# Kernel optimization log

Hardware: AMD Instinct MI355X
Metric: run time of the kernel (lower is better)

## Reference

```python
import jax, jax.numpy as jnp
import numpy as np

B, NPG, H, HEADS, L, E, IN_DIM, FREQ = 4, 256, 128, 4, 6, 65536, 5, 256
N = B * NPG
C = H // HEADS  # per-head channels = 32


def _w(key, shape, fan_in):
    return jax.random.normal(key, shape, jnp.float32) * (fan_in ** -0.5)


def _ln(x):  # LayerNorm, elementwise_affine=False, eps=1e-5
    mu = jnp.mean(x, axis=-1, keepdims=True)
    var = jnp.mean((x - mu) ** 2, axis=-1, keepdims=True)
    return (x - mu) / jnp.sqrt(var + 1e-5)


def setup_inputs() -> dict:
    key = jax.random.key(0)
    ks = jax.random.split(key, 40)
    x = jax.random.normal(ks[0], (N, IN_DIM), jnp.float32)
    # edges constrained within each graph
    kg = jnp.repeat(jnp.arange(B), E // B)
    src = jax.random.randint(ks[1], (E,), 0, NPG) + kg * NPG
    dst = jax.random.randint(ks[2], (E,), 0, NPG) + kg * NPG
    edge_index = jnp.stack([src, dst]).astype(jnp.int32)
    batch = jnp.repeat(jnp.arange(B), NPG).astype(jnp.int32)
    time_matrix = jax.random.normal(ks[3], (N, N), jnp.float32)
    p = {}
    p['Wn'] = _w(ks[4], (IN_DIM, H), IN_DIM); p['bn'] = jnp.zeros((H,), jnp.float32)
    p['Wee'] = _w(ks[5], (1, 1), 1); p['bee'] = jnp.zeros((1,), jnp.float32)
    p['Wt1'] = _w(ks[6], (FREQ, H), FREQ); p['bt1'] = jnp.zeros((H,), jnp.float32)
    p['Wt2'] = _w(ks[7], (H, H), H); p['bt2'] = jnp.zeros((H,), jnp.float32)
    p['Wa'] = _w(ks[8], (L, H, 4 * H), H); p['ba'] = jnp.zeros((L, 4 * H), jnp.float32)
    p['Wq'] = _w(ks[9], (L, H, H), H); p['bq'] = jnp.zeros((L, H), jnp.float32)
    p['Wk'] = _w(ks[10], (L, H, H), H); p['bk'] = jnp.zeros((L, H), jnp.float32)
    p['Wv'] = _w(ks[11], (L, H, H), H); p['bv'] = jnp.zeros((L, H), jnp.float32)
    p['We'] = _w(ks[12], (L, 1, H), 1)  # lin_edge, bias=False in PyG
    p['Wskip'] = _w(ks[13], (L, H, H), H); p['bskip'] = jnp.zeros((L, H), jnp.float32)
    p['Wf1'] = _w(ks[14], (L, H, 2 * H), H); p['bf1'] = jnp.zeros((L, 2 * H), jnp.float32)
    p['Wf2'] = _w(ks[15], (L, 2 * H, H), 2 * H); p['bf2'] = jnp.zeros((L, H), jnp.float32)
    p['Wb'] = _w(ks[16], (H, H, H), H); p['bb'] = jnp.zeros((H,), jnp.float32)
    p['Wm1'] = _w(ks[17], (H, H), H); p['bm1'] = jnp.zeros((H,), jnp.float32)
    p['Wm2'] = _w(ks[18], (H, 4), H); p['bm2'] = jnp.zeros((4,), jnp.float32)
    return {'x': x, 'edge_index': edge_index, 'batch': batch, 't': 50,
            'time_matrix': time_matrix, **p}


def reference(x, edge_index, batch, t, time_matrix,
              Wn, bn, Wee, bee, Wt1, bt1, Wt2, bt2,
              Wa, ba, Wq, bq, Wk, bk, Wv, bv, We, Wskip, bskip,
              Wf1, bf1, Wf2, bf2, Wb, bb, Wm1, bm1, Wm2, bm2):
    h = x @ Wn + bn  # [N,H]
    # sinusoidal timestep embedding (dim=FREQ)
    half = FREQ // 2
    freqs = jnp.exp(-jnp.log(jnp.float32(10000.0)) * jnp.arange(half, dtype=jnp.float32) / half)
    targs = jnp.float32(t) * freqs
    emb = jnp.concatenate([jnp.cos(targs), jnp.sin(targs)])[None, :]  # [1,FREQ]
    t_emb = jax.nn.silu(emb @ Wt1 + bt1) @ Wt2 + bt2  # [1,H]
    t_mod = jax.nn.silu(t_emb)

    src, dst = edge_index[0], edge_index[1]
    edge_attr = time_matrix[src, dst][:, None] @ Wee + bee  # [E,1]

    inv_sqrt_c = jnp.float32(1.0 / np.sqrt(C))
    for l in range(L):
        ss = t_mod @ Wa[l] + ba[l]  # [1,4H]
        sh_msa, sc_msa, sh_mlp, sc_mlp = jnp.split(ss, 4, axis=1)
        hn = _ln(h) * (1 + sc_msa) + sh_msa
        # TransformerConv: gather per-edge Q/K/V, softmax over incoming edges of dst
        q = (hn @ Wq[l] + bq[l]).reshape(N, HEADS, C)
        k = (hn @ Wk[l] + bk[l]).reshape(N, HEADS, C)
        v = (hn @ Wv[l] + bv[l]).reshape(N, HEADS, C)
        e = (edge_attr @ We[l]).reshape(E, HEADS, C)
        kj = k[src] + e
        alpha = jnp.sum(q[dst] * kj, axis=-1) * inv_sqrt_c  # [E,HEADS]
        m = jax.ops.segment_max(alpha, dst, num_segments=N)
        a = jnp.exp(alpha - m[dst])
        s = jax.ops.segment_sum(a, dst, num_segments=N)
        a = a / (s[dst] + 1e-16)
        msg = (v[src] + e) * a[..., None]  # [E,HEADS,C]
        attn_out = jax.ops.segment_sum(msg, dst, num_segments=N).reshape(N, H)
        attn_out = attn_out + hn @ Wskip[l] + bskip[l]  # root/skip connection
        h = h + attn_out
        hn = _ln(h) * (1 + sc_mlp) + sh_mlp
        h = h + (jax.nn.gelu(hn @ Wf1[l] + bf1[l], approximate=False) @ Wf2[l] + bf2[l])

    # to_dense_batch: all graphs have NPG nodes -> reshape, full mask
    hd = h.reshape(B, NPG, H)
    # nn.Bilinear: pair[b,i,j,o] = h[b,i] @ Wb[o] @ h[b,j] + bb[o]
    tmp = jnp.einsum('bik,okl->biol', hd, Wb)  # [B,n,H,H]
    pair = jnp.einsum('biol,bjl->bijo', tmp, hd) + bb  # [B,n,n,H]
    logits = jax.nn.silu(pair @ Wm1 + bm1) @ Wm2 + bm2  # [B,n,n,4]
    return logits
```

## Files before the change

kernel.cpp:

```cpp
#include <hip/hip_runtime.h>
#include <math.h>

#define N_NODES 1024
#define HDIM 128
#define EDGES 65536
#define LAYERS 6

typedef __attribute__((ext_vector_type(8))) short bf16x8;
typedef __attribute__((ext_vector_type(4))) float f32x4;

#define OFF_H     0
#define OFF_Q     131072
#define OFF_K     262144
#define OFF_V     393216
#define OFF_SKP   524288
#define OFF_G     655360
#define OFF_SS    917504
#define OFF_EA    920576
#define OFF_CVEC  986112
#define OFF_INT   986240
#define OFF_M     1054912
#define OFF_U     3152064
#define OFF_MT    11540672
#define OFF_HB    12589248
#define OFF_TMOD  12654784
#define OFF_WB    12654912

#define WM1T_OFF  786432

__device__ __forceinline__ float silu_f(float x) { return x / (1.f + expf(-x)); }
__device__ __forceinline__ float frcp(float x) { return __builtin_amdgcn_rcpf(x); }

__device__ __forceinline__ unsigned short f2bf(float f) {
    unsigned int u = __float_as_uint(f);
    u += 0x7FFFu + ((u >> 16) & 1u);
    return (unsigned short)(u >> 16);
}

__global__ __launch_bounds__(256) void k_ssf(const void* tptr,
    const float* __restrict__ Wt1, const float* __restrict__ bt1,
    const float* __restrict__ Wt2, const float* __restrict__ bt2,
    const float* __restrict__ bb, const float* __restrict__ Wm1, const float* __restrict__ bm1,
    const float* __restrict__ Wa, const float* __restrict__ ba,
    float* __restrict__ ss_all, float* __restrict__ cvec)
{
    __shared__ float emb_s[256];
    __shared__ float part[2][128];
    __shared__ float tmp1_s[128];
    __shared__ float tmod_s[128];
    int tid = threadIdx.x;
    int iv = *(const int*)tptr;
    float fv = __int_as_float(iv);
    float tval = (iv > -1000000 && iv < 1000000) ? (float)iv : fv;
    {
        int fi = tid & 127;
        float fr = expf(-logf(10000.f) * (float)fi / 128.f);
        float ta = tval * fr;
        emb_s[tid] = (tid < 128) ? cosf(ta) : sinf(ta);
    }
    __syncthreads();
    {
        int col = tid & 127, sl = tid >> 7;
        float p = 0.f;
#pragma unroll 8
        for (int i = sl * 128; i < sl * 128 + 128; i++) p += emb_s[i] * Wt1[i * 128 + col];
        part[sl][col] = p;
    }
    __syncthreads();
    if (tid < 128) tmp1_s[tid] = silu_f(bt1[tid] + part[0][tid] + part[1][tid]);
    __syncthreads();
    {
        int col = tid & 127, sl = tid >> 7;
        float p = 0.f;
#pragma unroll 8
        for (int i = sl * 64; i < sl * 64 + 64; i++) p += tmp1_s[i] * Wt2[i * 128 + col];
        part[sl][col] = p;
    }
    __syncthreads();
    if (tid < 128) tmod_s[tid] = silu_f(bt2[tid] + part[0][tid] + part[1][tid]);
    __syncthreads();
    {
        int idx = blockIdx.x * 256 + tid;
        int l = idx >> 9, j = idx & 511;
        float a = ba[l * 512 + j];
        const float* w = Wa + l * 65536 + j;
#pragma unroll 4
        for (int k = 0; k < 128; k++) a += tmod_s[k] * w[k * 512];
        ss_all[idx] = a;
    }
    if (blockIdx.x == 0) {
        {
            int col = tid & 127, sl = tid >> 7;
            float p = 0.f;
#pragma unroll 8
            for (int i = sl * 64; i < sl * 64 + 64; i++) p += bb[i] * Wm1[i * 128 + col];
            part[sl][col] = p;
        }
        __syncthreads();
        if (tid < 128) cvec[tid] = bm1[tid] + part[0][tid] + part[1][tid];
    }
}

__global__ __launch_bounds__(256) void k_wtrans(
    const float* __restrict__ Wq, const float* __restrict__ Wk,
    const float* __restrict__ Wv, const float* __restrict__ Wsk,
    const float* __restrict__ Wf1, const float* __restrict__ Wf2,
    const float* __restrict__ Wm1, short* __restrict__ WT)
{
    __shared__ __align__(16) short T[64][80];
    int t = blockIdx.x;
    int tid = threadIdx.x;
    const float* src; short* dst; int K, N, kt, nt;
    if (t < 96) {
        int mat = t >> 2, sub = t & 3;
        int l = mat >> 2, m = mat & 3;
        src = (m == 0 ? Wq : m == 1 ? Wk : m == 2 ? Wv : Wsk) + l * 16384;
        dst = WT + (size_t)mat * 16384;
        K = 128; N = 128; kt = sub >> 1; nt = sub & 1;
    } else if (t < 144) {
        int i = t - 96; int l = i >> 3, sub = i & 7;
        src = Wf1 + l * 32768;
        dst = WT + 24 * 16384 + (size_t)l * 32768;
        K = 128; N = 256; kt = sub & 1; nt = sub >> 1;
    } else if (t < 192) {
        int i = t - 144; int l = i >> 3, sub = i & 7;
        src = Wf2 + l * 32768;
        dst = WT + 24 * 16384 + 6 * 32768 + (size_t)l * 32768;
        K = 256; N = 128; kt = sub >> 1; nt = sub & 1;
    } else {
        int sub = t - 192;
        src = Wm1;
        dst = WT + WM1T_OFF;
        K = 128; N = 128; kt = sub >> 1; nt = sub & 1;
    }
    int k0 = kt * 64, n0 = nt * 64;
    for (int p = 0; p < 16; p++) {
        int idx = p * 256 + tid;
        int kk = idx >> 6, nn = idx & 63;
        T[nn][kk] = (short)f2bf(src[(k0 + kk) * N + n0 + nn]);
    }
    __syncthreads();
    for (int p = 0; p < 2; p++) {
        int idx = p * 256 + tid;
        int nn = idx >> 3, sq = idx & 7;
        *(int4*)&dst[(size_t)(n0 + nn) * K + k0 + sq * 8] = *(const int4*)&T[nn][sq * 8];
    }
}

__global__ __launch_bounds__(256) void k_inpedge(const float* __restrict__ x,
    const float* __restrict__ Wn, const float* __restrict__ bn, float* __restrict__ h,
    const int* __restrict__ ei, const float* __restrict__ tm,
    const float* __restrict__ Wee, const float* __restrict__ bee,
    float* __restrict__ ea, int* __restrict__ deg)
{
    int bid = blockIdx.x;
    int tid = threadIdx.x;
    if (bid < 512) {
        int idx = bid * 256 + tid;
        int i = idx >> 7, j = idx & 127;
        float acc = bn[j];
#pragma unroll
        for (int kk = 0; kk < 5; kk++) acc += x[i * 5 + kk] * Wn[kk * 128 + j];
        h[idx] = acc;
    } else {
        int e = (bid - 512) * 256 + tid;
        int s = ei[e], d = ei[EDGES + e];
        ea[e] = tm[s * N_NODES + d] * Wee[0] + bee[0];
        atomicAdd(&deg[d], 1);
    }
}

__global__ __launch_bounds__(1024) void k_scan(const int* __restrict__ deg, int* __restrict__ rowptr)
{
    __shared__ int tmp[1024];
    int tid = threadIdx.x;
    tmp[tid] = deg[tid];
    __syncthreads();
    for (int off = 1; off < 1024; off <<= 1) {
        int vv = (tid >= off) ? tmp[tid - off] : 0;
        __syncthreads();
        tmp[tid] += vv;
        __syncthreads();
    }
    rowptr[tid + 1] = tmp[tid];
    if (tid == 0) rowptr[0] = 0;
}

__global__ __launch_bounds__(256) void k_scatter(const int* __restrict__ ei,
    const int* __restrict__ rowptr, int* __restrict__ cursor, int* __restrict__ eorder)
{
    int e = blockIdx.x * 256 + threadIdx.x;
    int d = ei[EDGES + e];
    int pos = atomicAdd(&cursor[d], 1);
    eorder[rowptr[d] + pos] = e;
}

__global__ __launch_bounds__(128) void k_sort2(const int* __restrict__ rowptr,
    int* __restrict__ eorder, const int* __restrict__ ei, const float* __restrict__ ea,
    int* __restrict__ src_csr, float* __restrict__ ea_csr)
{
    __shared__ int key[256];
    int node = blockIdx.x;
    int tid = threadIdx.x;
    int beg = rowptr[node], end = rowptr[node + 1];
    int n = end - beg;
    if (n <= 256) {
        for (int i = tid; i < 256; i += 128) key[i] = (i < n) ? eorder[beg + i] : 0x7FFFFFFF;
        __syncthreads();
        for (int k = 2; k <= 256; k <<= 1) {
            for (int j = k >> 1; j > 0; j >>= 1) {
                int i = ((tid / j) * 2 * j) + (tid % j);
                int l = i + j;
                bool up = ((i & k) == 0);
                int a = key[i], b = key[l];
                if ((a > b) == up) { key[i] = b; key[l] = a; }
                __syncthreads();
            }
        }
        for (int i = tid; i < n; i += 128) {
            int e = key[i];
            src_csr[beg + i] = ei[e];
            ea_csr[beg + i] = ea[e];
        }
    } else {
        if (tid == 0) {
            for (int i = beg + 1; i < end; ++i) {
                int kk = eorder[i];
                int j = i - 1;
                while (j >= beg && eorder[j] > kk) { eorder[j + 1] = eorder[j]; --j; }
                eorder[j + 1] = kk;
            }
        }
        __syncthreads();
        for (int i = tid; i < n; i += 128) {
            int e = eorder[beg + i];
            src_csr[beg + i] = ei[e];
            ea_csr[beg + i] = ea[e];
        }
    }
}

__global__ __launch_bounds__(256) void k_qkvs(const float* __restrict__ h,
    const float* __restrict__ ss, const short* __restrict__ WT, int layer,
    const float* __restrict__ bq, const float* __restrict__ bk,
    const float* __restrict__ bv, const float* __restrict__ bsk,
    float* __restrict__ q, float* __restrict__ k, float* __restrict__ v, float* __restrict__ skp)
{
    __shared__ __align__(16) short As[32][136];
    __shared__ float shs[128], scs[128];
    int tid = threadIdx.x;
    int r0 = blockIdx.x * 32;
    int mat = blockIdx.y;
    if (tid < 128) { shs[tid] = ss[tid]; scs[tid] = ss[128 + tid]; }
    __syncthreads();
    {
        int row = tid >> 3, o = tid & 7;
        const float* hr = h + (size_t)(r0 + row) * 128 + o * 16;
        float s = 0.f, s2 = 0.f;
#pragma unroll
        for (int j = 0; j < 4; j++) {
            float4 vv = *(const float4*)&hr[j * 4];
            s += vv.x + vv.y + vv.z + vv.w;
            s2 += vv.x * vv.x + vv.y * vv.y + vv.z * vv.z + vv.w * vv.w;
        }
        s += __shfl_xor(s, 1, 64); s2 += __shfl_xor(s2, 1, 64);
        s += __shfl_xor(s, 2, 64); s2 += __shfl_xor(s2, 2, 64);
        s += __shfl_xor(s, 4, 64); s2 += __shfl_xor(s2, 4, 64);
        float mu = s * (1.f / 128.f);
        float var = s2 * (1.f / 128.f) - mu * mu;
        float rs = rsqrtf(var + 1e-5f);
#pragma unroll
        for (int j = 0; j < 4; j++) {
            float4 vv = *(const float4*)&hr[j * 4];
            int cb = o * 16 + j * 4;
            short4 o4;
            o4.x = (short)f2bf((vv.x - mu) * rs * (1.f + scs[cb])     + shs[cb]);
            o4.y = (short)f2bf((vv.y - mu) * rs * (1.f + scs[cb + 1]) + shs[cb + 1]);
            o4.z = (short)f2bf((vv.z - mu) * rs * (1.f + scs[cb + 2]) + shs[cb + 2]);
            o4.w = (short)f2bf((vv.w - mu) * rs * (1.f + scs[cb + 3]) + shs[cb + 3]);
            *(short4*)&As[row][cb] = o4;
        }
    }
    __syncthreads();
    int w = tid >> 6, lane = tid & 63, c = lane & 15, g = lane >> 4;
    const short* Wm = WT + (size_t)(layer * 4 + mat) * 16384;
    f32x4 acc[2][2] = {};
#pragma unroll
    for (int kq = 0; kq < 4; kq++) {
        int ko = kq * 32 + g * 8;
        bf16x8 a0 = *(const bf16x8*)&As[c][ko];
        bf16x8 a1 = *(const bf16x8*)&As[16 + c][ko];
#pragma unroll
        for (int nt = 0; nt < 2; nt++) {
            bf16x8 bfr = *(const bf16x8*)&Wm[(size_t)(w * 32 + nt * 16 + c) * 128 + ko];
            acc[0][nt] = __builtin_amdgcn_mfma_f32_16x16x32_bf16(a0, bfr, acc[0][nt], 0, 0, 0);
            acc[1][nt] = __builtin_amdgcn_mfma_f32_16x16x32_bf16(a1, bfr, acc[1][nt], 0, 0, 0);
        }
    }
    const float* bias; float* out;
    switch (mat) {
        case 0:  bias = bq;  out = q;   break;
        case 1:  bias = bk;  out = k;   break;
        case 2:  bias = bv;  out = v;   break;
        default: bias = bsk; out = skp; break;
    }
#pragma unroll
    for (int it = 0; it < 2; it++)
#pragma unroll
        for (int nt = 0; nt < 2; nt++) {
            int n = w * 32 + nt * 16 + c;
            float bv2 = bias[n];
#pragma unroll
            for (int r = 0; r < 4; r++) {
                int i = r0 + it * 16 + g * 4 + r;
                out[(size_t)i * 128 + n] = acc[it][nt][r] + bv2;
            }
        }
}

__global__ __launch_bounds__(256) void k_ffn(float* __restrict__ h,
    const short* __restrict__ WT, int layer,
    const float* __restrict__ bf1, const float* __restrict__ bf2,
    const float* __restrict__ ss2, short* __restrict__ hb, int last)
{
    __shared__ __align__(16) short As[16][136];
    __shared__ __align__(16) short Gs[16][264];
    __shared__ float shs[128], scs[128];
    int tid = threadIdx.x;
    int r0 = blockIdx.x * 16;
    if (tid < 128) { shs[tid] = ss2[tid]; scs[tid] = ss2[128 + tid]; }
    __syncthreads();
    {
        int row = tid >> 4, o = tid & 15;
        const float* hr = h + (size_t)(r0 + row) * 128 + o * 8;
        float s = 0.f, s2 = 0.f;
#pragma unroll
        for (int j = 0; j < 2; j++) {
            float4 vv = *(const float4*)&hr[j * 4];
            s += vv.x + vv.y + vv.z + vv.w;
            s2 += vv.x * vv.x + vv.y * vv.y + vv.z * vv.z + vv.w * vv.w;
        }
        s += __shfl_xor(s, 1, 64); s2 += __shfl_xor(s2, 1, 64);
        s += __shfl_xor(s, 2, 64); s2 += __shfl_xor(s2, 2, 64);
        s += __shfl_xor(s, 4, 64); s2 += __shfl_xor(s2, 4, 64);
        s += __shfl_xor(s, 8, 64); s2 += __shfl_xor(s2, 8, 64);
        float mu = s * (1.f / 128.f);
        float var = s2 * (1.f / 128.f) - mu * mu;
        float rs = rsqrtf(var + 1e-5f);
#pragma unroll
        for (int j = 0; j < 2; j++) {
            float4 vv = *(const float4*)&hr[j * 4];
            int cb = o * 8 + j * 4;
            short4 o4;
            o4.x = (short)f2bf((vv.x - mu) * rs * (1.f + scs[cb])     + shs[cb]);
            o4.y = (short)f2bf((vv.y - mu) * rs * (1.f + scs[cb + 1]) + shs[cb + 1]);
            o4.z = (short)f2bf((vv.z - mu) * rs * (1.f + scs[cb + 2]) + shs[cb + 2]);
            o4.w = (short)f2bf((vv.w - mu) * rs * (1.f + scs[cb + 3]) + shs[cb + 3]);
            *(short4*)&As[row][cb] = o4;
        }
    }
    __syncthreads();
    int w = tid >> 6, lane = tid & 63, c = lane & 15, g = lane >> 4;
    const short* W1 = WT + 24 * 16384 + (size_t)layer * 32768;
    const short* W2 = WT + 24 * 16384 + 6 * 32768 + (size_t)layer * 32768;
    {
        f32x4 acc[4] = {};
#pragma unroll
        for (int kq = 0; kq < 4; kq++) {
            int ko = kq * 32 + g * 8;
            bf16x8 a0 = *(const bf16x8*)&As[c][ko];
#pragma unroll
            for (int nt = 0; nt < 4; nt++) {
                bf16x8 bfr = *(const bf16x8*)&W1[(size_t)(w * 64 + nt * 16 + c) * 128 + ko];
                acc[nt] = __builtin_amdgcn_mfma_f32_16x16x32_bf16(a0, bfr, acc[nt], 0, 0, 0);
            }
        }
#pragma unroll
        for (int nt = 0; nt < 4; nt++) {
            int n = w * 64 + nt * 16 + c;
            float bv = bf1[n];
#pragma unroll
            for (int r = 0; r < 4; r++) {
                float y = acc[nt][r] + bv;
                float gl = 0.5f * y * (1.f + erff(y * 0.70710678118654752f));
                Gs[g * 4 + r][n] = (short)f2bf(gl);
            }
        }
    }
    __syncthreads();
    {
        f32x4 acc2[2] = {};
#pragma unroll
        for (int kq = 0; kq < 8; kq++) {
            int ko = kq * 32 + g * 8;
            bf16x8 a0 = *(const bf16x8*)&Gs[c][ko];
#pragma unroll
            for (int nt2 = 0; nt2 < 2; nt2++) {
                bf16x8 bfr = *(const bf16x8*)&W2[(size_t)(w * 32 + nt2 * 16 + c) * 256 + ko];
                acc2[nt2] = __builtin_amdgcn_mfma_f32_16x16x32_bf16(a0, bfr, acc2[nt2], 0, 0, 0);
            }
        }
#pragma unroll
        for (int nt2 = 0; nt2 < 2; nt2++) {
            int n = w * 32 + nt2 * 16 + c;
            float bv = bf2[n];
#pragma unroll
            for (int r = 0; r < 4; r++) {
                int i = r0 + g * 4 + r;
                float nv = h[(size_t)i * 128 + n] + acc2[nt2][r] + bv;
                h[(size_t)i * 128 + n] = nv;
                if (last) hb[(size_t)i * 128 + n] = (short)f2bf(nv);
            }
        }
    }
}

__global__ __launch_bounds__(256) void k_attn(const float* __restrict__ q,
    const float* __restrict__ k, const float* __restrict__ v,
    const float* __restrict__ skp, float* __restrict__ h,
    const int* __restrict__ src_csr, const float* __restrict__ ea_csr,
    const float* __restrict__ We_l, const int* __restrict__ rowptr)
{
    __shared__ float ms[3][64], ssb[3][64], a0s[3][64], a1s[3][64];
    int tid = threadIdx.x;
    int wid = tid >> 6;
    int lane = tid & 63;
    int node = blockIdx.x;
    int c0 = lane * 2;
    float2 q2 = *(const float2*)&q[node * 128 + c0];
    float we0 = We_l[c0], we1 = We_l[c0 + 1];
    int beg = rowptr[node], end = rowptr[node + 1];
    int n = end - beg;
    int tb = beg + (n * wid) / 4;
    int te = beg + (n * (wid + 1)) / 4;
    float m = -INFINITY, s = 0.f, a0 = 0.f, a1 = 0.f;
    const float isc = 0.17677669529663687f;

    int t = tb;
    for (; t + 3 < te; t += 4) {
        int sn0 = src_csr[t],     sn1 = src_csr[t + 1];
        int sn2 = src_csr[t + 2], sn3 = src_csr[t + 3];
        float e0 = ea_csr[t],     e1 = ea_csr[t + 1];
        float e2 = ea_csr[t + 2], e3 = ea_csr[t + 3];
        float2 k0 = *(const float2*)&k[sn0 * 128 + c0];
        float2 k1 = *(const float2*)&k[sn1 * 128 + c0];
        float2 k2 = *(const float2*)&k[sn2 * 128 + c0];
        float2 k3 = *(const float2*)&k[sn3 * 128 + c0];
        float2 v0 = *(const float2*)&v[sn0 * 128 + c0];
        float2 v1 = *(const float2*)&v[sn1 * 128 + c0];
        float2 v2 = *(const float2*)&v[sn2 * 128 + c0];
        float2 v3 = *(const float2*)&v[sn3 * 128 + c0];
        float p0 = q2.x * (k0.x + e0 * we0) + q2.y * (k0.y + e0 * we1);
        float p1 = q2.x * (k1.x + e1 * we0) + q2.y * (k1.y + e1 * we1);
        float p2 = q2.x * (k2.x + e2 * we0) + q2.y * (k2.y + e2 * we1);
        float p3 = q2.x * (k3.x + e3 * we0) + q2.y * (k3.y + e3 * we1);
        p0 += __shfl_xor(p0, 1, 16); p1 += __shfl_xor(p1, 1, 16);
        p2 += __shfl_xor(p2, 1, 16); p3 += __shfl_xor(p3, 1, 16);
        p0 += __shfl_xor(p0, 2, 16); p1 += __shfl_xor(p1, 2, 16);
        p2 += __shfl_xor(p2, 2, 16); p3 += __shfl_xor(p3, 2, 16);
        p0 += __shfl_xor(p0, 4, 16); p1 += __shfl_xor(p1, 4, 16);
        p2 += __shfl_xor(p2, 4, 16); p3 += __shfl_xor(p3, 4, 16);
        p0 += __shfl_xor(p0, 8, 16); p1 += __shfl_xor(p1, 8, 16);
        p2 += __shfl_xor(p2, 8, 16); p3 += __shfl_xor(p3, 8, 16);
        {
            float al = p0 * isc;
            float mn = fmaxf(m, al);
            float scale = __expf(m - mn), wq = __expf(al - mn);
            s = s * scale + wq;
            a0 = a0 * scale + wq * (v0.x + e0 * we0);
            a1 = a1 * scale + wq * (v0.y + e0 * we1);
            m = mn;
        }
        {
            float al = p1 * isc;
            float mn = fmaxf(m, al);
            float scale = __expf(m - mn), wq = __expf(al - mn);
            s = s * scale + wq;
            a0 = a0 * scale + wq * (v1.x + e1 * we0);
            a1 = a1 * scale + wq * (v1.y + e1 * we1);
            m = mn;
        }
        {
            float al = p2 * isc;
            float mn = fmaxf(m, al);
            float scale = __expf(m - mn), wq = __expf(al - mn);
            s = s * scale + wq;
            a0 = a0 * scale + wq * (v2.x + e2 * we0);
            a1 = a1 * scale + wq * (v2.y + e2 * we1);
            m = mn;
        }
        {
            float al = p3 * isc;
            float mn = fmaxf(m, al);
            float scale = __expf(m - mn), wq = __expf(al - mn);
            s = s * scale + wq;
            a0 = a0 * scale + wq * (v3.x + e3 * we0);
            a1 = a1 * scale + wq * (v3.y + e3 * we1);
            m = mn;
        }
    }
    for (; t < te; ++t) {
        int sn = src_csr[t];
        float eav = ea_csr[t];
        float2 kv = *(const float2*)&k[sn * 128 + c0];
        float2 vv = *(const float2*)&v[sn * 128 + c0];
        float part = q2.x * (kv.x + eav * we0) + q2.y * (kv.y + eav * we1);
        part += __shfl_xor(part, 1, 16);
        part += __shfl_xor(part, 2, 16);
        part += __shfl_xor(part, 4, 16);
        part += __shfl_xor(part, 8, 16);
        float alpha = part * isc;
        float mn = fmaxf(m, alpha);
        float scale = __expf(m - mn), wq = __expf(alpha - mn);
        s = s * scale + wq;
        a0 = a0 * scale + wq * (vv.x + eav * we0);
        a1 = a1 * scale + wq * (vv.y + eav * we1);
        m = mn;
    }
    if (wid > 0) {
        ms[wid - 1][lane] = m; ssb[wid - 1][lane] = s;
        a0s[wid - 1][lane] = a0; a1s[wid - 1][lane] = a1;
    }
    __syncthreads();
    if (wid == 0) {
#pragma unroll
        for (int p = 0; p < 3; p++) {
            float mB = ms[p][lane], sB = ssb[p][lane];
            float b0 = a0s[p][lane], b1 = a1s[p][lane];
            float mm = fmaxf(m, mB);
            float eA = (m  > -1e30f) ? __expf(m  - mm) : 0.f;
            float eB = (mB > -1e30f) ? __expf(mB - mm) : 0.f;
            s = s * eA + sB * eB;
            a0 = a0 * eA + b0 * eB;
            a1 = a1 * eA + b1 * eB;
            m = mm;
        }
        float inv = (s > 0.f) ? 1.f / (s + 1e-16f) : 0.f;
        int o = node * 128 + c0;
        h[o]     += skp[o]     + a0 * inv;
        h[o + 1] += skp[o + 1] + a1 * inv;
    }
}

__global__ __launch_bounds__(256) void k_mprep(const float* __restrict__ Wb,
    const short* __restrict__ WT, float* __restrict__ M)
{
    __shared__ __align__(16) short Bls[128][136];
    int tid = threadIdx.x;
    int k = blockIdx.x;
    const short* Wm1T = WT + WM1T_OFF;
    {
        int lq = (tid & 31) * 4;
        int ob = tid >> 5;
        for (int it = 0; it < 16; it++) {
            int o = it * 8 + ob;
            float4 vv = *(const float4*)&Wb[(size_t)o * 16384 + k * 128 + lq];
            Bls[lq][o]     = (short)f2bf(vv.x);
            Bls[lq + 1][o] = (short)f2bf(vv.y);
            Bls[lq + 2][o] = (short)f2bf(vv.z);
            Bls[lq + 3][o] = (short)f2bf(vv.w);
        }
    }
    __syncthreads();
    int w = tid >> 6, lane = tid & 63, c = lane & 15, g = lane >> 4;
    f32x4 acc[2][8] = {};
#pragma unroll
    for (int kq = 0; kq < 4; kq++) {
        int ko = kq * 32 + g * 8;
        bf16x8 a0 = *(const bf16x8*)&Wm1T[(size_t)(w * 32 + c) * 128 + ko];
        bf16x8 a1 = *(const bf16x8*)&Wm1T[(size_t)(w * 32 + 16 + c) * 128 + ko];
#pragma unroll
        for (int nt = 0; nt < 8; nt++) {
            bf16x8 b = *(const bf16x8*)&Bls[nt * 16 + c][ko];
            acc[0][nt] = __builtin_amdgcn_mfma_f32_16x16x32_bf16(a0, b, acc[0][nt], 0, 0, 0);
            acc[1][nt] = __builtin_amdgcn_mfma_f32_16x16x32_bf16(a1, b, acc[1][nt], 0, 0, 0);
        }
    }
    float* Mk = M + (size_t)k * 16384;
#pragma unroll
    for (int it = 0; it < 2; it++)
#pragma unroll
        for (int nt = 0; nt < 8; nt++)
#pragma unroll
            for (int r = 0; r < 4; r++) {
                int m = w * 32 + it * 16 + g * 4 + r;
                int l = nt * 16 + c;
                Mk[m * 128 + l] = acc[it][nt][r];
            }
}

__global__ __launch_bounds__(256) void k_mtrans(const float* __restrict__ M,
                                                short* __restrict__ Mt)
{
    __shared__ __align__(16) short Ts[64][136];
    int tid = threadIdx.x;
    int n0 = blockIdx.x * 64;
    for (int p = 0; p < 32; p++) {
        int idx = p * 256 + tid;
        int k = idx >> 6, nn = idx & 63;
        Ts[nn][k] = (short)f2bf(M[(size_t)k * 16384 + n0 + nn]);
    }
    __syncthreads();
    for (int p = 0; p < 4; p++) {
        int idx = p * 256 + tid;
        int nn = idx >> 4, s = idx & 15;
        *(int4*)&Mt[(size_t)(n0 + nn) * 128 + s * 8] = *(const int4*)&Ts[nn][s * 8];
    }
}

__global__ __launch_bounds__(256) void k_p1(const short* __restrict__ hb,
    const short* __restrict__ Mt, short* __restrict__ U)
{
    __shared__ __align__(16) short As[128][72];
    __shared__ __align__(16) short Bs[128][72];
    int tid = threadIdx.x;
    int n0 = blockIdx.x * 128;
    int i0 = blockIdx.y * 128;
    int w = tid >> 6, lane = tid & 63, c = lane & 15, g = lane >> 4;
    f32x4 acc[2][8] = {};
    for (int kh = 0; kh < 2; kh++) {
        __syncthreads();
        for (int idx = tid; idx < 1024; idx += 256) {
            int r = idx >> 3, s = idx & 7;
            *(int4*)&As[r][s * 8] = *(const int4*)&hb[(i0 + r) * 128 + kh * 64 + s * 8];
            *(int4*)&Bs[r][s * 8] = *(const int4*)&Mt[(size_t)(n0 + r) * 128 + kh * 64 + s * 8];
        }
        __syncthreads();
#pragma unroll
        for (int kk = 0; kk < 2; kk++) {
            int ko = kk * 32 + g * 8;
            bf16x8 a0 = *(const bf16x8*)&As[w * 32 + c][ko];
            bf16x8 a1 = *(const bf16x8*)&As[w * 32 + 16 + c][ko];
#pragma unroll
            for (int nt = 0; nt < 8; nt++) {
                bf16x8 b = *(const bf16x8*)&Bs[nt * 16 + c][ko];
                acc[0][nt] = __builtin_amdgcn_mfma_f32_16x16x32_bf16(a0, b, acc[0][nt], 0, 0, 0);
                acc[1][nt] = __builtin_amdgcn_mfma_f32_16x16x32_bf16(a1, b, acc[1][nt], 0, 0, 0);
            }
        }
    }
#pragma unroll
    for (int it = 0; it < 2; it++)
#pragma unroll
        for (int nt = 0; nt < 8; nt++)
#pragma unroll
            for (int r = 0; r < 4; r++) {
                int i = i0 + w * 32 + it * 16 + g * 4 + r;
                int n = n0 + nt * 16 + c;
                U[(size_t)i * 16384 + n] = (short)f2bf(acc[it][nt][r]);
            }
}

__global__ __launch_bounds__(256) void k_p2(const short* __restrict__ hb,
    const short* __restrict__ U, const float* __restrict__ cvec,
    const float* __restrict__ Wm2, const float* __restrict__ bm2,
    float* __restrict__ out)
{
    __shared__ __align__(16) short Us[128][136];
    __shared__ float cvs[128];
    __shared__ float w2s[128][4];
    int tid = threadIdx.x;
    int i = blockIdx.x;
    int jb = blockIdx.y;
    int b = i >> 8;
    int w = tid >> 6, lane = tid & 63, c = lane & 15, g = lane >> 4;
    if (tid < 128) {
        cvs[tid] = cvec[tid];
        *(float4*)&w2s[tid][0] = *(const float4*)&Wm2[tid * 4];
    }
    bf16x8 hf[2][4];
    {
        const short* hrow = hb + (size_t)(b * 256 + jb * 128 + w * 32 + c) * 128;
#pragma unroll
        for (int jt = 0; jt < 2; jt++)
#pragma unroll
            for (int kq = 0; kq < 4; kq++)
                hf[jt][kq] = *(const bf16x8*)(hrow + jt * 16 * 128 + kq * 32 + g * 8);
    }
    for (int idx = tid; idx < 2048; idx += 256) {
        int r = idx >> 4, s = idx & 15;
        *(int4*)&Us[r][s * 8] = *(const int4*)&U[(size_t)i * 16384 + r * 128 + s * 8];
    }
    __syncthreads();
    f32x4 acc[2][8] = {};
#pragma unroll
    for (int kq = 0; kq < 4; kq++) {
        int ko = kq * 32 + g * 8;
#pragma unroll
        for (int mt = 0; mt < 8; mt++) {
            bf16x8 uv = *(const bf16x8*)&Us[mt * 16 + c][ko];
            acc[0][mt] = __builtin_amdgcn_mfma_f32_16x16x32_bf16(uv, hf[0][kq], acc[0][mt], 0, 0, 0);
            acc[1][mt] = __builtin_amdgcn_mfma_f32_16x16x32_bf16(uv, hf[1][kq], acc[1][mt], 0, 0, 0);
        }
    }
    float4 bmv = *(const float4*)&bm2[0];
#pragma unroll
    for (int jt = 0; jt < 2; jt++) {
        float p0 = 0.f, p1 = 0.f, p2 = 0.f, p3 = 0.f;
#pragma unroll
        for (int mt = 0; mt < 8; mt++) {
#pragma unroll
            for (int r = 0; r < 4; r++) {
                int m = mt * 16 + g * 4 + r;
                float y = acc[jt][mt][r] + cvs[m];
                float sv = y * frcp(1.f + __expf(-y));
                p0 += sv * w2s[m][0]; p1 += sv * w2s[m][1];
                p2 += sv * w2s[m][2]; p3 += sv * w2s[m][3];
            }
        }
        p0 += __shfl_xor(p0, 16, 64); p1 += __shfl_xor(p1, 16, 64);
        p2 += __shfl_xor(p2, 16, 64); p3 += __shfl_xor(p3, 16, 64);
        p0 += __shfl_xor(p0, 32, 64); p1 += __shfl_xor(p1, 32, 64);
        p2 += __shfl_xor(p2, 32, 64); p3 += __shfl_xor(p3, 32, 64);
        if (g == 0) {
            int j = jb * 128 + w * 32 + jt * 16 + c;
            float4 o4 = { p0 + bmv.x, p1 + bmv.y, p2 + bmv.z, p3 + bmv.w };
            *(float4*)&out[((size_t)i * 256 + j) * 4] = o4;
        }
    }
}

extern "C" void kernel_launch(void* const* d_in, const int* in_sizes, int n_in,
                              void* d_out, int out_size, void* d_ws, size_t ws_size,
                              hipStream_t stream)
{
    const float* x   = (const float*)d_in[0];
    const int*   ei  = (const int*)d_in[1];
    const void*  tptr= d_in[3];
    const float* tm  = (const float*)d_in[4];
    const float* Wn  = (const float*)d_in[5];
    const float* bn  = (const float*)d_in[6];
    const float* Wee = (const float*)d_in[7];
    const float* bee = (const float*)d_in[8];
    const float* Wt1 = (const float*)d_in[9];
    const float* bt1 = (const float*)d_in[10];
    const float* Wt2 = (const float*)d_in[11];
    const float* bt2 = (const float*)d_in[12];
    const float* Wa  = (const float*)d_in[13];
    const float* ba  = (const float*)d_in[14];
    const float* Wq  = (const float*)d_in[15];
    const float* bq  = (const float*)d_in[16];
    const float* Wk  = (const float*)d_in[17];
    const float* bk  = (const float*)d_in[18];
    const float* Wv  = (const float*)d_in[19];
    const float* bv  = (const float*)d_in[20];
    const float* We  = (const float*)d_in[21];
    const float* Wsk = (const float*)d_in[22];
    const float* bsk = (const float*)d_in[23];
    const float* Wf1 = (const float*)d_in[24];
    const float* bf1 = (const float*)d_in[25];
    const float* Wf2 = (const float*)d_in[26];
    const float* bf2 = (const float*)d_in[27];
    const float* Wb  = (const float*)d_in[28];
    const float* bb  = (const float*)d_in[29];
    const float* Wm1 = (const float*)d_in[30];
    const float* bm1 = (const float*)d_in[31];
    const float* Wm2 = (const float*)d_in[32];
    const float* bm2 = (const float*)d_in[33];
    float* out = (float*)d_out;
    float* ws = (float*)d_ws;

    float* h    = ws + OFF_H;
    float* qb   = ws + OFF_Q;
    float* kb   = ws + OFF_K;
    float* vb   = ws + OFF_V;
    float* skp  = ws + OFF_SKP;
    float* ss   = ws + OFF_SS;
    float* ea   = ws + OFF_EA;
    float* cvec = ws + OFF_CVEC;
    int* iws    = (int*)(ws + OFF_INT);
    int* deg    = iws;
    int* cursor = iws + 1024;
    int* rowptr = iws + 2048;
    int* eorder = iws + 3073;
    int* src_csr   = (int*)(ws + OFF_G);
    float* ea_csr  = ws + OFF_G + 65536;
    float* Mst  = ws + OFF_M;
    short* Ub   = (short*)(ws + OFF_U);
    short* Mtb  = (short*)(ws + OFF_MT);
    short* hbb  = (short*)(ws + OFF_HB);
    short* WT   = (short*)(ws + OFF_WB);

    hipMemsetAsync(deg, 0, 2048 * sizeof(int), stream);
    k_ssf<<<12, 256, 0, stream>>>(tptr, Wt1, bt1, Wt2, bt2, bb, Wm1, bm1, Wa, ba, ss, cvec);
    k_wtrans<<<196, 256, 0, stream>>>(Wq, Wk, Wv, Wsk, Wf1, Wf2, Wm1, WT);
    k_inpedge<<<768, 256, 0, stream>>>(x, Wn, bn, h, ei, tm, Wee, bee, ea, deg);
    k_scan<<<1, 1024, 0, stream>>>(deg, rowptr);
    k_scatter<<<256, 256, 0, stream>>>(ei, rowptr, cursor, eorder);
    k_sort2<<<1024, 128, 0, stream>>>(rowptr, eorder, ei, ea, src_csr, ea_csr);

    for (int l = 0; l < LAYERS; l++) {
        const float* ssl = ss + l * 512;
        k_qkvs<<<dim3(32, 4), 256, 0, stream>>>(h, ssl, WT, l,
            bq + l * 128, bk + l * 128, bv + l * 128, bsk + l * 128,
            qb, kb, vb, skp);
        k_attn<<<1024, 256, 0, stream>>>(qb, kb, vb, skp, h, src_csr, ea_csr,
                                         We + l * 128, rowptr);
        k_ffn<<<64, 256, 0, stream>>>(h, WT, l, bf1 + l * 256, bf2 + l * 128,
                                      ssl + 256, hbb, l == LAYERS - 1);
    }

    k_mprep<<<128, 256, 0, stream>>>(Wb, WT, Mst);
    k_mtrans<<<256, 256, 0, stream>>>(Mst, Mtb);
    k_p1<<<dim3(128, 8), 256, 0, stream>>>(hbb, Mtb, Ub);
    k_p2<<<dim3(1024, 2), 256, 0, stream>>>(hbb, Ub, cvec, Wm2, bm2, out);
}
```

Measured before the change: 266.3 us.

## Store K/V in bf16, restructure QKVS blocking and merge P2 column halves

The K and V projections are now written as bf16, and the attention gather reads them as bf16 and widens to float. This halves the gather traffic in the edge loop, at the cost of lower precision in K and V. The QKVS kernel now gives each wave one of the four matrices over 16 rows, instead of using a grid dimension per matrix, so the LayerNorm is computed once per row tile rather than four times. k_p2 drops its second grid dimension: each block loads the U tile once and loops over all 256 columns, removing duplicate U loads at the cost of fewer blocks.

Result: slower. 272.8 us (+2.4%).

```diff
diff --git a/kernel.cpp b/kernel.cpp
--- a/kernel.cpp
+++ b/kernel.cpp
@@ -23,7 +23,6 @@
 #define OFF_U     3152064
 #define OFF_MT    11540672
 #define OFF_HB    12589248
-#define OFF_TMOD  12654784
 #define OFF_WB    12654912
 
 #define WM1T_OFF  786432
@@ -35,6 +34,9 @@
     unsigned int u = __float_as_uint(f);
     u += 0x7FFFu + ((u >> 16) & 1u);
     return (unsigned short)(u >> 16);
+}
+__device__ __forceinline__ float bf2f(unsigned short s) {
+    return __uint_as_float(((unsigned int)s) << 16);
 }
 
 __global__ __launch_bounds__(256) void k_ssf(const void* tptr,
@@ -244,91 +246,14 @@
     const float* __restrict__ ss, const short* __restrict__ WT, int layer,
     const float* __restrict__ bq, const float* __restrict__ bk,
     const float* __restrict__ bv, const float* __restrict__ bsk,
-    float* __restrict__ q, float* __restrict__ k, float* __restrict__ v, float* __restrict__ skp)
-{
-    __shared__ __align__(16) short As[32][136];
+    float* __restrict__ q, short* __restrict__ kb16, short* __restrict__ vb16,
+    float* __restrict__ skp)
+{
+    __shared__ __align__(16) short As[16][136];
     __shared__ float shs[128], scs[128];
     int tid = threadIdx.x;
-    int r0 = blockIdx.x * 32;
-    int mat = blockIdx.y;
+    int r0 = blockIdx.x * 16;
     if (tid < 128) { shs[tid] = ss[tid]; scs[tid] = ss[128 + tid]; }
-    __syncthreads();
-    {
-        int row = tid >> 3, o = tid & 7;
-        const float* hr = h + (size_t)(r0 + row) * 128 + o * 16;
-        float s = 0.f, s2 = 0.f;
-#pragma unroll
-        for (int j = 0; j < 4; j++) {
-            float4 vv = *(const float4*)&hr[j * 4];
-            s += vv.x + vv.y + vv.z + vv.w;
-            s2 += vv.x * vv.x + vv.y * vv.y + vv.z * vv.z + vv.w * vv.w;
-        }
-        s += __shfl_xor(s, 1, 64); s2 += __shfl_xor(s2, 1, 64);
-        s += __shfl_xor(s, 2, 64); s2 += __shfl_xor(s2, 2, 64);
-        s += __shfl_xor(s, 4, 64); s2 += __shfl_xor(s2, 4, 64);
-        float mu = s * (1.f / 128.f);
-        float var = s2 * (1.f / 128.f) - mu * mu;
-        float rs = rsqrtf(var + 1e-5f);
-#pragma unroll
-        for (int j = 0; j < 4; j++) {
-            float4 vv = *(const float4*)&hr[j * 4];
-            int cb = o * 16 + j * 4;
-            short4 o4;
-            o4.x = (short)f2bf((vv.x - mu) * rs * (1.f + scs[cb])     + shs[cb]);
-            o4.y = (short)f2bf((vv.y - mu) * rs * (1.f + scs[cb + 1]) + shs[cb + 1]);
-            o4.z = (short)f2bf((vv.z - mu) * rs * (1.f + scs[cb + 2]) + shs[cb + 2]);
-            o4.w = (short)f2bf((vv.w - mu) * rs * (1.f + scs[cb + 3]) + shs[cb + 3]);
-            *(short4*)&As[row][cb] = o4;
-        }
-    }
-    __syncthreads();
-    int w = tid >> 6, lane = tid & 63, c = lane & 15, g = lane >> 4;
-    const short* Wm = WT + (size_t)(layer * 4 + mat) * 16384;
-    f32x4 acc[2][2] = {};
-#pragma unroll
-    for (int kq = 0; kq < 4; kq++) {
-        int ko = kq * 32 + g * 8;
-        bf16x8 a0 = *(const bf16x8*)&As[c][ko];
-        bf16x8 a1 = *(const bf16x8*)&As[16 + c][ko];
-#pragma unroll
-        for (int nt = 0; nt < 2; nt++) {
-            bf16x8 bfr = *(const bf16x8*)&Wm[(size_t)(w * 32 + nt * 16 + c) * 128 + ko];
-            acc[0][nt] = __builtin_amdgcn_mfma_f32_16x16x32_bf16(a0, bfr, acc[0][nt], 0, 0, 0);
-            acc[1][nt] = __builtin_amdgcn_mfma_f32_16x16x32_bf16(a1, bfr, acc[1][nt], 0, 0, 0);
-        }
-    }
-    const float* bias; float* out;
-    switch (mat) {
-        case 0:  bias = bq;  out = q;   break;
-        case 1:  bias = bk;  out = k;   break;
-        case 2:  bias = bv;  out = v;   break;
-        default: bias = bsk; out = skp; break;
-    }
-#pragma unroll
-    for (int it = 0; it < 2; it++)
-#pragma unroll
-        for (int nt = 0; nt < 2; nt++) {
-            int n = w * 32 + nt * 16 + c;
-            float bv2 = bias[n];
-#pragma unroll
-            for (int r = 0; r < 4; r++) {
-                int i = r0 + it * 16 + g * 4 + r;
-                out[(size_t)i * 128 + n] = acc[it][nt][r] + bv2;
-            }
-        }
-}
-
-__global__ __launch_bounds__(256) void k_ffn(float* __restrict__ h,
-    const short* __restrict__ WT, int layer,
-    const float* __restrict__ bf1, const float* __restrict__ bf2,
-    const float* __restrict__ ss2, short* __restrict__ hb, int last)
-{
-    __shared__ __align__(16) short As[16][136];
-    __shared__ __align__(16) short Gs[16][264];
-    __shared__ float shs[128], scs[128];
-    int tid = threadIdx.x;
-    int r0 = blockIdx.x * 16;
-    if (tid < 128) { shs[tid] = ss2[tid]; scs[tid] = ss2[128 + tid]; }
     __syncthreads();
     {
         int row = tid >> 4, o = tid & 15;
@@ -361,6 +286,100 @@
     }
     __syncthreads();
     int w = tid >> 6, lane = tid & 63, c = lane & 15, g = lane >> 4;
+    const short* Wm = WT + (size_t)(layer * 4 + w) * 16384;
+    f32x4 acc[8] = {};
+#pragma unroll
+    for (int kq = 0; kq < 4; kq++) {
+        int ko = kq * 32 + g * 8;
+        bf16x8 a0 = *(const bf16x8*)&As[c][ko];
+#pragma unroll
+        for (int nt = 0; nt < 8; nt++) {
+            bf16x8 bfr = *(const bf16x8*)&Wm[(size_t)(nt * 16 + c) * 128 + ko];
+            acc[nt] = __builtin_amdgcn_mfma_f32_16x16x32_bf16(a0, bfr, acc[nt], 0, 0, 0);
+        }
+    }
+    if (w == 0) {
+#pragma unroll
+        for (int nt = 0; nt < 8; nt++) {
+            int n = nt * 16 + c;
+            float bv2 = bq[n];
+#pragma unroll
+            for (int r = 0; r < 4; r++)
+                q[(size_t)(r0 + g * 4 + r) * 128 + n] = acc[nt][r] + bv2;
+        }
+    } else if (w == 1) {
+#pragma unroll
+        for (int nt = 0; nt < 8; nt++) {
+            int n = nt * 16 + c;
+            float bv2 = bk[n];
+#pragma unroll
+            for (int r = 0; r < 4; r++)
+                kb16[(size_t)(r0 + g * 4 + r) * 128 + n] = (short)f2bf(acc[nt][r] + bv2);
+        }
+    } else if (w == 2) {
+#pragma unroll
+        for (int nt = 0; nt < 8; nt++) {
+            int n = nt * 16 + c;
+            float bv2 = bv[n];
+#pragma unroll
+            for (int r = 0; r < 4; r++)
+                vb16[(size_t)(r0 + g * 4 + r) * 128 + n] = (short)f2bf(acc[nt][r] + bv2);
+        }
+    } else {
+#pragma unroll
+        for (int nt = 0; nt < 8; nt++) {
+            int n = nt * 16 + c;
+            float bv2 = bsk[n];
+#pragma unroll
+            for (int r = 0; r < 4; r++)
+                skp[(size_t)(r0 + g * 4 + r) * 128 + n] = acc[nt][r] + bv2;
+        }
+    }
+}
+
+__global__ __launch_bounds__(256) void k_ffn(float* __restrict__ h,
+    const short* __restrict__ WT, int layer,
+    const float* __restrict__ bf1, const float* __restrict__ bf2,
+    const float* __restrict__ ss2, short* __restrict__ hb, int last)
+{
+    __shared__ __align__(16) short As[16][136];
+    __shared__ __align__(16) short Gs[16][264];
+    __shared__ float shs[128], scs[128];
+    int tid = threadIdx.x;
+    int r0 = blockIdx.x * 16;
+    if (tid < 128) { shs[tid] = ss2[tid]; scs[tid] = ss2[128 + tid]; }
+    __syncthreads();
+    {
+        int row = tid >> 4, o = tid & 15;
+        const float* hr = h + (size_t)(r0 + row) * 128 + o * 8;
+        float s = 0.f, s2 = 0.f;
+#pragma unroll
+        for (int j = 0; j < 2; j++) {
+            float4 vv = *(const float4*)&hr[j * 4];
+            s += vv.x + vv.y + vv.z + vv.w;
+            s2 += vv.x * vv.x + vv.y * vv.y + vv.z * vv.z + vv.w * vv.w;
+        }
+        s += __shfl_xor(s, 1, 64); s2 += __shfl_xor(s2, 1, 64);
+        s += __shfl_xor(s, 2, 64); s2 += __shfl_xor(s2, 2, 64);
+        s += __shfl_xor(s, 4, 64); s2 += __shfl_xor(s2, 4, 64);
+        s += __shfl_xor(s, 8, 64); s2 += __shfl_xor(s2, 8, 64);
+        float mu = s * (1.f / 128.f);
+        float var = s2 * (1.f / 128.f) - mu * mu;
+        float rs = rsqrtf(var + 1e-5f);
+#pragma unroll
+        for (int j = 0; j < 2; j++) {
+            float4 vv = *(const float4*)&hr[j * 4];
+            int cb = o * 8 + j * 4;
+            short4 o4;
+            o4.x = (short)f2bf((vv.x - mu) * rs * (1.f + scs[cb])     + shs[cb]);
+            o4.y = (short)f2bf((vv.y - mu) * rs * (1.f + scs[cb + 1]) + shs[cb + 1]);
+            o4.z = (short)f2bf((vv.z - mu) * rs * (1.f + scs[cb + 2]) + shs[cb + 2]);
+            o4.w = (short)f2bf((vv.w - mu) * rs * (1.f + scs[cb + 3]) + shs[cb + 3]);
+            *(short4*)&As[row][cb] = o4;
+        }
+    }
+    __syncthreads();
+    int w = tid >> 6, lane = tid & 63, c = lane & 15, g = lane >> 4;
     const short* W1 = WT + 24 * 16384 + (size_t)layer * 32768;
     const short* W2 = WT + 24 * 16384 + 6 * 32768 + (size_t)layer * 32768;
     {
@@ -416,7 +435,7 @@
 }
 
 __global__ __launch_bounds__(256) void k_attn(const float* __restrict__ q,
-    const float* __restrict__ k, const float* __restrict__ v,
+    const short* __restrict__ kb16, const short* __restrict__ vb16,
     const float* __restrict__ skp, float* __restrict__ h,
     const int* __restrict__ src_csr, const float* __restrict__ ea_csr,
     const float* __restrict__ We_l, const int* __restrict__ rowptr)
@@ -442,18 +461,18 @@
         int sn2 = src_csr[t + 2], sn3 = src_csr[t + 3];
         float e0 = ea_csr[t],     e1 = ea_csr[t + 1];
         float e2 = ea_csr[t + 2], e3 = ea_csr[t + 3];
-        float2 k0 = *(const float2*)&k[sn0 * 128 + c0];
-        float2 k1 = *(const float2*)&k[sn1 * 128 + c0];
-        float2 k2 = *(const float2*)&k[sn2 * 128 + c0];
-        float2 k3 = *(const float2*)&k[sn3 * 128 + c0];
-        float2 v0 = *(const float2*)&v[sn0 * 128 + c0];
-        float2 v1 = *(const float2*)&v[sn1 * 128 + c0];
-        float2 v2 = *(const float2*)&v[sn2 * 128 + c0];
-        float2 v3 = *(const float2*)&v[sn3 * 128 + c0];
-        float p0 = q2.x * (k0.x + e0 * we0) + q2.y * (k0.y + e0 * we1);
-        float p1 = q2.x * (k1.x + e1 * we0) + q2.y * (k1.y + e1 * we1);
-        float p2 = q2.x * (k2.x + e2 * we0) + q2.y * (k2.y + e2 * we1);
-        float p3 = q2.x * (k3.x + e3 * we0) + q2.y * (k3.y + e3 * we1);
+        ushort2 ku0 = *(const ushort2*)&kb16[sn0 * 128 + c0];
+        ushort2 ku1 = *(const ushort2*)&kb16[sn1 * 128 + c0];
+        ushort2 ku2 = *(const ushort2*)&kb16[sn2 * 128 + c0];
+        ushort2 ku3 = *(const ushort2*)&kb16[sn3 * 128 + c0];
+        ushort2 vu0 = *(const ushort2*)&vb16[sn0 * 128 + c0];
+        ushort2 vu1 = *(const ushort2*)&vb16[sn1 * 128 + c0];
+        ushort2 vu2 = *(const ushort2*)&vb16[sn2 * 128 + c0];
+        ushort2 vu3 = *(const ushort2*)&vb16[sn3 * 128 + c0];
+        float p0 = q2.x * (bf2f(ku0.x) + e0 * we0) + q2.y * (bf2f(ku0.y) + e0 * we1);
+        float p1 = q2.x * (bf2f(ku1.x) + e1 * we0) + q2.y * (bf2f(ku1.y) + e1 * we1);
+        float p2 = q2.x * (bf2f(ku2.x) + e2 * we0) + q2.y * (bf2f(ku2.y) + e2 * we1);
+        float p3 = q2.x * (bf2f(ku3.x) + e3 * we0) + q2.y * (bf2f(ku3.y) + e3 * we1);
         p0 += __shfl_xor(p0, 1, 16); p1 += __shfl_xor(p1, 1, 16);
         p2 += __shfl_xor(p2, 1, 16); p3 += __shfl_xor(p3, 1, 16);
         p0 += __shfl_xor(p0, 2, 16); p1 += __shfl_xor(p1, 2, 16);
@@ -467,8 +486,8 @@
             float mn = fmaxf(m, al);
             float scale = __expf(m - mn), wq = __expf(al - mn);
             s = s * scale + wq;
-            a0 = a0 * scale + wq * (v0.x + e0 * we0);
-            a1 = a1 * scale + wq * (v0.y + e0 * we1);
+            a0 = a0 * scale + wq * (bf2f(vu0.x) + e0 * we0);
+            a1 = a1 * scale + wq * (bf2f(vu0.y) + e0 * we1);
             m = mn;
         }
         {
@@ -476,8 +495,8 @@
             float mn = fmaxf(m, al);
             float scale = __expf(m - mn), wq = __expf(al - mn);
             s = s * scale + wq;
-            a0 = a0 * scale + wq * (v1.x + e1 * we0);
-            a1 = a1 * scale + wq * (v1.y + e1 * we1);
+            a0 = a0 * scale + wq * (bf2f(vu1.x) + e1 * we0);
+            a1 = a1 * scale + wq * (bf2f(vu1.y) + e1 * we1);
             m = mn;
         }
         {
@@ -485,8 +504,8 @@
             float mn = fmaxf(m, al);
             float scale = __expf(m - mn), wq = __expf(al - mn);
             s = s * scale + wq;
-            a0 = a0 * scale + wq * (v2.x + e2 * we0);
-            a1 = a1 * scale + wq * (v2.y + e2 * we1);
+            a0 = a0 * scale + wq * (bf2f(vu2.x) + e2 * we0);
+            a1 = a1 * scale + wq * (bf2f(vu2.y) + e2 * we1);
             m = mn;
         }
         {
@@ -494,17 +513,17 @@
             float mn = fmaxf(m, al);
             float scale = __expf(m - mn), wq = __expf(al - mn);
             s = s * scale + wq;
-            a0 = a0 * scale + wq * (v3.x + e3 * we0);
-            a1 = a1 * scale + wq * (v3.y + e3 * we1);
+            a0 = a0 * scale + wq * (bf2f(vu3.x) + e3 * we0);
+            a1 = a1 * scale + wq * (bf2f(vu3.y) + e3 * we1);
             m = mn;
         }
     }
     for (; t < te; ++t) {
         int sn = src_csr[t];
         float eav = ea_csr[t];
-        float2 kv = *(const float2*)&k[sn * 128 + c0];
-        float2 vv = *(const float2*)&v[sn * 128 + c0];
-        float part = q2.x * (kv.x + eav * we0) + q2.y * (kv.y + eav * we1);
+        ushort2 ku = *(const ushort2*)&kb16[sn * 128 + c0];
+        ushort2 vu = *(const ushort2*)&vb16[sn * 128 + c0];
+        float part = q2.x * (bf2f(ku.x) + eav * we0) + q2.y * (bf2f(ku.y) + eav * we1);
         part += __shfl_xor(part, 1, 16);
         part += __shfl_xor(part, 2, 16);
         part += __shfl_xor(part, 4, 16);
@@ -513,8 +532,8 @@
         float mn = fmaxf(m, alpha);
         float scale = __expf(m - mn), wq = __expf(alpha - mn);
         s = s * scale + wq;
-        a0 = a0 * scale + wq * (vv.x + eav * we0);
-        a1 = a1 * scale + wq * (vv.y + eav * we1);
+        a0 = a0 * scale + wq * (bf2f(vu.x) + eav * we0);
+        a1 = a1 * scale + wq * (bf2f(vu.y) + eav * we1);
         m = mn;
     }
     if (wid > 0) {
@@ -661,48 +680,43 @@
     __shared__ float w2s[128][4];
     int tid = threadIdx.x;
     int i = blockIdx.x;
-    int jb = blockIdx.y;
     int b = i >> 8;
     int w = tid >> 6, lane = tid & 63, c = lane & 15, g = lane >> 4;
     if (tid < 128) {
         cvs[tid] = cvec[tid];
         *(float4*)&w2s[tid][0] = *(const float4*)&Wm2[tid * 4];
     }
-    bf16x8 hf[2][4];
-    {
-        const short* hrow = hb + (size_t)(b * 256 + jb * 128 + w * 32 + c) * 128;
-#pragma unroll
-        for (int jt = 0; jt < 2; jt++)
-#pragma unroll
-            for (int kq = 0; kq < 4; kq++)
-                hf[jt][kq] = *(const bf16x8*)(hrow + jt * 16 * 128 + kq * 32 + g * 8);
-    }
     for (int idx = tid; idx < 2048; idx += 256) {
         int r = idx >> 4, s = idx & 15;
         *(int4*)&Us[r][s * 8] = *(const int4*)&U[(size_t)i * 16384 + r * 128 + s * 8];
     }
     __syncthreads();
-    f32x4 acc[2][8] = {};
-#pragma unroll
-    for (int kq = 0; kq < 4; kq++) {
-        int ko = kq * 32 + g * 8;
-#pragma unroll
-        for (int mt = 0; mt < 8; mt++) {
-            bf16x8 uv = *(const bf16x8*)&Us[mt * 16 + c][ko];
-            acc[0][mt] = __builtin_amdgcn_mfma_f32_16x16x32_bf16(uv, hf[0][kq], acc[0][mt], 0, 0, 0);
-            acc[1][mt] = __builtin_amdgcn_mfma_f32_16x16x32_bf16(uv, hf[1][kq], acc[1][mt], 0, 0, 0);
-        }
-    }
     float4 bmv = *(const float4*)&bm2[0];
 #pragma unroll
-    for (int jt = 0; jt < 2; jt++) {
+    for (int jt = 0; jt < 4; jt++) {
+        int jbase = w * 64 + jt * 16;
+        bf16x8 hf[4];
+        const short* hrow = hb + (size_t)(b * 256 + jbase + c) * 128;
+#pragma unroll
+        for (int kq = 0; kq < 4; kq++)
+            hf[kq] = *(const bf16x8*)(hrow + kq * 32 + g * 8);
+        f32x4 acc[8] = {};
+#pragma unroll
+        for (int kq = 0; kq < 4; kq++) {
+            int ko = kq * 32 + g * 8;
+#pragma unroll
+            for (int mt = 0; mt < 8; mt++) {
+                bf16x8 uv = *(const bf16x8*)&Us[mt * 16 + c][ko];
+                acc[mt] = __builtin_amdgcn_mfma_f32_16x16x32_bf16(uv, hf[kq], acc[mt], 0, 0, 0);
+            }
+        }
         float p0 = 0.f, p1 = 0.f, p2 = 0.f, p3 = 0.f;
 #pragma unroll
         for (int mt = 0; mt < 8; mt++) {
 #pragma unroll
             for (int r = 0; r < 4; r++) {
                 int m = mt * 16 + g * 4 + r;
-                float y = acc[jt][mt][r] + cvs[m];
+                float y = acc[mt][r] + cvs[m];
                 float sv = y * frcp(1.f + __expf(-y));
                 p0 += sv * w2s[m][0]; p1 += sv * w2s[m][1];
                 p2 += sv * w2s[m][2]; p3 += sv * w2s[m][3];
@@ -713,7 +727,7 @@
         p0 += __shfl_xor(p0, 32, 64); p1 += __shfl_xor(p1, 32, 64);
         p2 += __shfl_xor(p2, 32, 64); p3 += __shfl_xor(p3, 32, 64);
         if (g == 0) {
-            int j = jb * 128 + w * 32 + jt * 16 + c;
+            int j = jbase + c;
             float4 o4 = { p0 + bmv.x, p1 + bmv.y, p2 + bmv.z, p3 + bmv.w };
             *(float4*)&out[((size_t)i * 256 + j) * 4] = o4;
         }
@@ -762,8 +776,8 @@
 
     float* h    = ws + OFF_H;
     float* qb   = ws + OFF_Q;
-    float* kb   = ws + OFF_K;
-    float* vb   = ws + OFF_V;
+    short* kb16 = (short*)(ws + OFF_K);
+    short* vb16 = (short*)(ws + OFF_V);
     float* skp  = ws + OFF_SKP;
     float* ss   = ws + OFF_SS;
     float* ea   = ws + OFF_EA;
@@ -791,10 +805,10 @@
 
     for (int l = 0; l < LAYERS; l++) {
         const float* ssl = ss + l * 512;
-        k_qkvs<<<dim3(32, 4), 256, 0, stream>>>(h, ssl, WT, l,
+        k_qkvs<<<64, 256, 0, stream>>>(h, ssl, WT, l,
             bq + l * 128, bk + l * 128, bv + l * 128, bsk + l * 128,
-            qb, kb, vb, skp);
-        k_attn<<<1024, 256, 0, stream>>>(qb, kb, vb, skp, h, src_csr, ea_csr,
+            qb, kb16, vb16, skp);
+        k_attn<<<1024, 256, 0, stream>>>(qb, kb16, vb16, skp, h, src_csr, ea_csr,
                                          We + l * 128, rowptr);
         k_ffn<<<64, 256, 0, stream>>>(h, WT, l, bf1 + l * 256, bf2 + l * 128,
                                       ssl + 256, hbb, l == LAYERS - 1);
@@ -803,5 +817,5 @@
     k_mprep<<<128, 256, 0, stream>>>(Wb, WT, Mst);
     k_mtrans<<<256, 256, 0, stream>>>(Mst, Mtb);
     k_p1<<<dim3(128, 8), 256, 0, stream>>>(hbb, Mtb, Ub);
-    k_p2<<<dim3(1024, 2), 256, 0, stream>>>(hbb, Ub, cvec, Wm2, bm2, out);
-}
+    k_p2<<<1024, 256, 0, stream>>>(hbb, Ub, cvec, Wm2, bm2, out);
+}
```
